# Kernel optimization log

Hardware: AMD Instinct MI355X
Metric: run time of the kernel (lower is better)

## Reference

```python
import jax, jax.numpy as jnp
import numpy as np

B, CD, NF, V, D = 16384, 13, 26, 100000, 64
BOT = [256, 128]
TOP = [512, 256, 128]
NUM_EMB = NF + 1            # 27 (bottom output + 26 categorical)
NUM_INTER = NUM_EMB * (NUM_EMB - 1) // 2  # 351
TOP_IN = NUM_INTER + NUM_EMB * D          # 2079
BN_INV = 1.0 / np.sqrt(1.0 + 1e-5)        # eval-mode BatchNorm: running_mean=0, running_var=1


def _lin(key, fan_in, fan_out):
    kw, kb = jax.random.split(key)
    s = 1.0 / np.sqrt(fan_in)
    W = jax.random.uniform(kw, (fan_in, fan_out), minval=-s, maxval=s, dtype=jnp.float32)
    b = jax.random.uniform(kb, (fan_out,), minval=-s, maxval=s, dtype=jnp.float32)
    return W, b


def setup_inputs() -> dict:
    key = jax.random.key(0)
    ks = jax.random.split(key, 16)
    continuous = jax.random.normal(ks[0], (B, CD), dtype=jnp.float32)
    cat_idx = jax.random.randint(ks[1], (B, NF), 0, V, dtype=jnp.int32)
    emb_tables = jax.random.normal(ks[2], (NF, V, D), dtype=jnp.float32)  # nn.Embedding init ~ N(0,1)
    W1, b1 = _lin(ks[3], CD, BOT[0]);   g1 = jnp.ones((BOT[0],)); be1 = jnp.zeros((BOT[0],))
    W2, b2 = _lin(ks[4], BOT[0], BOT[1]); g2 = jnp.ones((BOT[1],)); be2 = jnp.zeros((BOT[1],))
    W3, b3 = _lin(ks[5], BOT[1], D)
    W4, b4 = _lin(ks[6], TOP_IN, TOP[0]); g4 = jnp.ones((TOP[0],)); be4 = jnp.zeros((TOP[0],))
    W5, b5 = _lin(ks[7], TOP[0], TOP[1]); g5 = jnp.ones((TOP[1],)); be5 = jnp.zeros((TOP[1],))
    W6, b6 = _lin(ks[8], TOP[1], TOP[2]); g6 = jnp.ones((TOP[2],)); be6 = jnp.zeros((TOP[2],))
    W7, b7 = _lin(ks[9], TOP[2], 1)
    return dict(continuous=continuous, cat_idx=cat_idx, emb_tables=emb_tables,
                W1=W1, b1=b1, g1=g1, be1=be1, W2=W2, b2=b2, g2=g2, be2=be2, W3=W3, b3=b3,
                W4=W4, b4=b4, g4=g4, be4=be4, W5=W5, b5=b5, g5=g5, be5=be5,
                W6=W6, b6=b6, g6=g6, be6=be6, W7=W7, b7=b7)


def _bn(x, g, b):
    # eval-mode BatchNorm1d with running_mean=0, running_var=1
    return g * (x * BN_INV) + b


def reference(continuous, cat_idx, emb_tables,
              W1, b1, g1, be1, W2, b2, g2, be2, W3, b3,
              W4, b4, g4, be4, W5, b5, g5, be5, W6, b6, g6, be6, W7, b7):
    # Bottom MLP: 13 -> 256 -> 128 -> 64
    h = jax.nn.relu(_bn(continuous @ W1 + b1, g1, be1))
    h = jax.nn.relu(_bn(h @ W2 + b2, g2, be2))
    bottom = h @ W3 + b3                         # [B, D]

    # Embedding gather: one table per categorical feature
    emb = emb_tables[jnp.arange(NF), cat_idx]    # [B, NF, D]
    all_emb = jnp.concatenate([bottom[:, None, :], emb], axis=1)  # [B, 27, D]

    # Pairwise dot-product interactions via one bmm + triu gather
    Z = jnp.einsum('bnd,bmd->bnm', all_emb, all_emb)              # [B, 27, 27]
    iu, ju = np.triu_indices(NUM_EMB, k=1)                        # row-major i<j (matches torch loop order)
    inter = Z[:, iu, ju]                                          # [B, 351]

    top_in = jnp.concatenate([inter, all_emb.reshape(all_emb.shape[0], -1)], axis=1)  # [B, 2079]

    # Top MLP: 2079 -> 512 -> 256 -> 128 -> 1
    t = jax.nn.relu(_bn(top_in @ W4 + b4, g4, be4))
    t = jax.nn.relu(_bn(t @ W5 + b5, g5, be5))
    t = jax.nn.relu(_bn(t @ W6 + b6, g6, be6))
    scores = t @ W7 + b7                                          # [B, 1]
    return scores
```

## Files before the change

### kernel.cpp

```cpp
#include <hip/hip_runtime.h>
#include <stdint.h>
#include <stddef.h>

#define BATCH   16384
#define CDIM    13
#define NFEAT   26
#define VROWS   100000
#define EDIM    64
#define NEMB    27
#define NINTER  351
#define TOPIN   2079
#define KP4     2112
#define BN_INVF 0.9999950000374997f

typedef __attribute__((ext_vector_type(8)))  __bf16 bf16x8;
typedef __attribute__((ext_vector_type(4)))  float  f32x4;
typedef __attribute__((ext_vector_type(16))) float  f32x16;
typedef __attribute__((ext_vector_type(4)))  uint32_t uint4v;

__device__ __forceinline__ uint32_t f2bf(float f){
  uint32_t u = __float_as_uint(f);
  return (u + 0x7fffu + ((u >> 16) & 1u)) >> 16;
}
__device__ __forceinline__ float bf2f(uint32_t h){ return __uint_as_float(h << 16); }
__device__ __forceinline__ uint32_t pack2(float a, float b){
  return f2bf(a) | (f2bf(b) << 16);
}
__device__ __forceinline__ void async_load16(const void* g, void* l){
  __builtin_amdgcn_global_load_lds(
      (const __attribute__((address_space(1))) uint32_t*)g,
      (__attribute__((address_space(3))) uint32_t*)l, 16, 0, 0);
}
__device__ __forceinline__ int rswz(int row){ return ((row ^ (row >> 3)) & 7) << 3; }

__device__ __forceinline__ void transpose_tile(
    float (*tile)[65], const float* __restrict__ src, unsigned short* __restrict__ dst,
    int K, int N, int Kpad, int remap, int kb, int nb){
  int k0 = kb*64, n0 = nb*64, t = threadIdx.x;
  int srcBase = remap ? ((k0 < 1728) ? (k0 + 351) : (k0 - 1728)) : k0;
  #pragma unroll 4
  for(int p = 0; p < 16; p++){
    int kr = p*4 + (t >> 6), nc = t & 63;
    float v = 0.f;
    if(k0 + kr < K && (n0 + nc) < N) v = src[(size_t)(srcBase + kr) * N + n0 + nc];
    tile[kr][nc] = v;
  }
  __syncthreads();
  #pragma unroll 4
  for(int p = 0; p < 16; p++){
    int nr = p*4 + (t >> 6), kc = t & 63;
    if(k0 + kc < Kpad && (n0 + nr) < N)
      dst[(size_t)(n0 + nr) * Kpad + k0 + kc] = (unsigned short)f2bf(tile[kc][nr]);
  }
}

__global__ __launch_bounds__(256) void prep(
    const float* __restrict__ W1, const float* __restrict__ W2, const float* __restrict__ W3,
    const float* __restrict__ W4, const float* __restrict__ W5, const float* __restrict__ W6,
    unsigned short* __restrict__ W1t, unsigned short* __restrict__ W2t,
    unsigned short* __restrict__ W3t, unsigned short* __restrict__ W4t,
    unsigned short* __restrict__ W5t, unsigned short* __restrict__ W6t){
  __shared__ float tile[64][65];
  int bid = blockIdx.x;
  if(bid < 264){ transpose_tile(tile, W4, W4t, TOPIN, 512, KP4, 1, bid % 33, bid / 33); }
  else if(bid < 296){ int r = bid-264; transpose_tile(tile, W5, W5t, 512, 256, 512, 0, r % 8, r / 8); }
  else if(bid < 304){ int r = bid-296; transpose_tile(tile, W6, W6t, 256, 128, 256, 0, r % 4, r / 4); }
  else if(bid < 312){ int r = bid-304; transpose_tile(tile, W2, W2t, 256, 128, 256, 0, r % 4, r / 4); }
  else if(bid < 314){ int r = bid-312; transpose_tile(tile, W3, W3t, 128, 64, 128, 0, r, 0); }
  else               { int r = bid-314; transpose_tile(tile, W1, W1t, CDIM, 256, 32, 0, 0, r); }
}

__global__ __launch_bounds__(256) void bottom_interact(
    const float* __restrict__ cont, const int* __restrict__ cat_idx,
    const float* __restrict__ emb,
    const unsigned short* __restrict__ W1t, const unsigned short* __restrict__ W2t,
    const unsigned short* __restrict__ W3t,
    const float* __restrict__ b1, const float* __restrict__ g1, const float* __restrict__ be1,
    const float* __restrict__ b2, const float* __restrict__ g2, const float* __restrict__ be2,
    const float* __restrict__ b3,
    unsigned short* __restrict__ top_in){
  __shared__ unsigned short h1hi[16*256];
  __shared__ unsigned short h1lo[16*256];
  __shared__ unsigned short h2hi[16*128];
  __shared__ unsigned short h2lo[16*128];
  __shared__ unsigned short bot_s[16*64];
  __shared__ unsigned short inter_s[16][352];
  int t = threadIdx.x, w = t >> 6, l = t & 63;
  int m0 = blockIdx.x * 16;
  int lr = l & 15, lg = l >> 4, lk = lg * 8;
  int r = l & 31, h = l >> 5;
  bool activeB = (r >= 1 && r < NEMB);

  int idx4[4];
  #pragma unroll
  for(int s = 0; s < 4; s++){
    int b = m0 + w*4 + s;
    idx4[s] = activeB ? cat_idx[b*NFEAT + (r-1)] : 0;
  }

  bf16x8 axh, axl;
  {
    uint32_t uh[4], ul[4];
    #pragma unroll
    for(int p = 0; p < 4; p++){
      float x0 = 0.f, x1 = 0.f;
      int k0 = lk + 2*p;
      if(k0 < CDIM)     x0 = cont[(size_t)(m0 + lr)*CDIM + k0];
      if(k0 + 1 < CDIM) x1 = cont[(size_t)(m0 + lr)*CDIM + k0 + 1];
      uint32_t h0 = f2bf(x0), h1b = f2bf(x1);
      uh[p] = h0 | (h1b << 16);
      ul[p] = f2bf(x0 - bf2f(h0)) | (f2bf(x1 - bf2f(h1b)) << 16);
    }
    uint4v vh, vl;
    #pragma unroll
    for(int e = 0; e < 4; e++){ vh[e] = uh[e]; vl[e] = ul[e]; }
    axh = __builtin_bit_cast(bf16x8, vh);
    axl = __builtin_bit_cast(bf16x8, vl);
  }

  {
    #pragma unroll
    for(int nt = 0; nt < 4; nt++){
      int n = w*64 + nt*16 + lr;
      bf16x8 bw = *(const bf16x8*)(W1t + (size_t)n*32 + lk);
      f32x4 acc;
      #pragma unroll
      for(int e = 0; e < 4; e++) acc[e] = 0.f;
      acc = __builtin_amdgcn_mfma_f32_16x16x32_bf16(axh, bw, acc, 0, 0, 0);
      acc = __builtin_amdgcn_mfma_f32_16x16x32_bf16(axl, bw, acc, 0, 0, 0);
      float sc = g1[n]*BN_INVF, bo = be1[n], bi = b1[n];
      #pragma unroll
      for(int q = 0; q < 4; q++){
        int ro = lg*4 + q;
        float y = fmaxf(sc*(acc[q] + bi) + bo, 0.f);
        uint32_t hb = f2bf(y);
        int idx = ro*256 + (n ^ rswz(ro));
        h1hi[idx] = (unsigned short)hb;
        h1lo[idx] = (unsigned short)f2bf(y - bf2f(hb));
      }
    }
  }
  __syncthreads();

  {
    f32x4 acc[2];
    #pragma unroll
    for(int nt = 0; nt < 2; nt++)
      #pragma unroll
      for(int e = 0; e < 4; e++) acc[nt][e] = 0.f;
    for(int ks = 0; ks < 8; ks++){
      bf16x8 bw[2];
      #pragma unroll
      for(int nt = 0; nt < 2; nt++){
        int n = w*32 + nt*16 + lr;
        bw[nt] = *(const bf16x8*)(W2t + (size_t)n*256 + ks*32 + lk);
      }
      int ai = lr*256 + ((ks*32 + lk) ^ rswz(lr));
      bf16x8 ah = *(const bf16x8*)(h1hi + ai);
      bf16x8 al = *(const bf16x8*)(h1lo + ai);
      #pragma unroll
      for(int nt = 0; nt < 2; nt++){
        acc[nt] = __builtin_amdgcn_mfma_f32_16x16x32_bf16(ah, bw[nt], acc[nt], 0, 0, 0);
        acc[nt] = __builtin_amdgcn_mfma_f32_16x16x32_bf16(al, bw[nt], acc[nt], 0, 0, 0);
      }
    }
    #pragma unroll
    for(int nt = 0; nt < 2; nt++){
      int n = w*32 + nt*16 + lr;
      float sc = g2[n]*BN_INVF, bo = be2[n], bi = b2[n];
      #pragma unroll
      for(int q = 0; q < 4; q++){
        int ro = lg*4 + q;
        float y = fmaxf(sc*(acc[nt][q] + bi) + bo, 0.f);
        uint32_t hb = f2bf(y);
        int idx = ro*128 + (n ^ rswz(ro));
        h2hi[idx] = (unsigned short)hb;
        h2lo[idx] = (unsigned short)f2bf(y - bf2f(hb));
      }
    }
  }
  __syncthreads();

  {
    f32x4 acc;
    #pragma unroll
    for(int e = 0; e < 4; e++) acc[e] = 0.f;
    int n = w*16 + lr;
    for(int ks = 0; ks < 4; ks++){
      bf16x8 bw = *(const bf16x8*)(W3t + (size_t)n*128 + ks*32 + lk);
      int ai = lr*128 + ((ks*32 + lk) ^ rswz(lr));
      bf16x8 ah = *(const bf16x8*)(h2hi + ai);
      bf16x8 al = *(const bf16x8*)(h2lo + ai);
      acc = __builtin_amdgcn_mfma_f32_16x16x32_bf16(ah, bw, acc, 0, 0, 0);
      acc = __builtin_amdgcn_mfma_f32_16x16x32_bf16(al, bw, acc, 0, 0, 0);
    }
    float bi = b3[n];
    #pragma unroll
    for(int q = 0; q < 4; q++){
      int ro = lg*4 + q;
      bot_s[ro*64 + n] = (unsigned short)f2bf(acc[q] + bi);
    }
  }
  __syncthreads();

  float4 raw[8];
  if(activeB){
    const float* src = emb + ((size_t)(r-1)*VROWS + (size_t)idx4[0])*64;
    #pragma unroll
    for(int p = 0; p < 4; p++){
      raw[2*p]   = *(const float4*)(src + h*8 + p*16);
      raw[2*p+1] = *(const float4*)(src + h*8 + p*16 + 4);
    }
  }
  #pragma unroll
  for(int s = 0; s < 4; s++){
    int sb = w*4 + s;
    int b = m0 + sb;
    uint4v q[4];
    if(r == 0){
      #pragma unroll
      for(int p = 0; p < 4; p++)
        q[p] = *(const uint4v*)(bot_s + sb*64 + h*8 + p*16);
    } else if(activeB){
      #pragma unroll
      for(int p = 0; p < 4; p++){
        q[p][0] = pack2(raw[2*p].x, raw[2*p].y); q[p][1] = pack2(raw[2*p].z, raw[2*p].w);
        q[p][2] = pack2(raw[2*p+1].x, raw[2*p+1].y); q[p][3] = pack2(raw[2*p+1].z, raw[2*p+1].w);
      }
    } else {
      #pragma unroll
      for(int p = 0; p < 4; p++){ q[p][0]=0; q[p][1]=0; q[p][2]=0; q[p][3]=0; }
    }
    if(s < 3 && activeB){
      const float* src = emb + ((size_t)(r-1)*VROWS + (size_t)idx4[s+1])*64;
      #pragma unroll
      for(int p = 0; p < 4; p++){
        raw[2*p]   = *(const float4*)(src + h*8 + p*16);
        raw[2*p+1] = *(const float4*)(src + h*8 + p*16 + 4);
      }
    }
    if(r < NEMB){
      #pragma unroll
      for(int p = 0; p < 4; p++)
        *(uint4v*)(top_in + (size_t)b*KP4 + r*64 + h*8 + p*16) = q[p];
    }
    f32x16 acc;
    #pragma unroll
    for(int i = 0; i < 16; i++) acc[i] = 0.f;
    #pragma unroll
    for(int p = 0; p < 4; p++){
      bf16x8 a = __builtin_bit_cast(bf16x8, q[p]);
      acc = __builtin_amdgcn_mfma_f32_32x32x16_bf16(a, a, acc, 0, 0, 0);
    }
    if(r < NEMB){
      #pragma unroll
      for(int qq = 0; qq < 16; qq++){
        int i = (qq & 3) + 8*(qq >> 2) + 4*h;
        if(i < r){
          int p = i*(53 - i)/2 + (r - i - 1);
          inter_s[sb][p] = (unsigned short)f2bf(acc[qq]);
        }
      }
    }
    asm volatile("s_waitcnt lgkmcnt(0)" ::: "memory");
    size_t basei = (size_t)b*KP4 + 1728;
    for(int t0 = l; t0 < 176; t0 += 64){
      uint32_t lo = inter_s[sb][2*t0];
      uint32_t hi = (2*t0 + 1 < NINTER) ? (uint32_t)inter_s[sb][2*t0 + 1] : 0u;
      *(uint32_t*)(top_in + basei + 2*t0) = lo | (hi << 16);
    }
    if(l < 16) *(uint32_t*)(top_in + (size_t)b*KP4 + 2080 + 2*l) = 0;
  }
}

template<int KSTEPS, int NB>
__global__ __launch_bounds__(512, 2) void gemm_deep(
    const unsigned short* __restrict__ A, int sA,
    const unsigned short* __restrict__ Bw, int sB,
    const float* __restrict__ bias, const float* __restrict__ gg,
    const float* __restrict__ be,
    unsigned short* __restrict__ out, int sOut){
  __shared__ char smem[3*49152];
  int nwg = gridDim.x;
  int bid = blockIdx.x;
  int lin = (bid & 7) * (nwg >> 3) + (bid >> 3);
  int m0 = (lin / NB) * 256, n0 = (lin % NB) * 128;
  int t = threadIdx.x, w = t >> 6, l = t & 63;
  int wr = (w >> 1) * 64, wc = (w & 1) * 64;
  f32x4 acc[4][4];
  #pragma unroll
  for(int i = 0; i < 4; i++)
    #pragma unroll
    for(int j = 0; j < 4; j++)
      #pragma unroll
      for(int e = 0; e < 4; e++) acc[i][j][e] = 0.f;

  const unsigned short* g[6];
  int ldsOff[6];
  #pragma unroll
  for(int i = 0; i < 6; i++){
    if(i < 4){
      int o = i*8192 + t*16;
      int row = o >> 7;
      int cb  = (o & 127) ^ ((row & 7) << 4);
      g[i] = A + (size_t)(m0 + row)*sA + (cb >> 1);
      ldsOff[i] = o;
    } else {
      int o = (i-4)*8192 + t*16;
      int row = o >> 7;
      int cb  = (o & 127) ^ ((row & 7) << 4);
      g[i] = Bw + (size_t)(n0 + row)*sB + (cb >> 1);
      ldsOff[i] = 32768 + o;
    }
  }
  int lr = l & 15;
  int o1 = ((l >> 4) * 16) ^ ((l & 7) << 4);

  #pragma unroll
  for(int i = 0; i < 6; i++) async_load16(g[i], smem + ldsOff[i]);
  #pragma unroll
  for(int i = 0; i < 6; i++) async_load16(g[i] + 64, smem + 49152 + ldsOff[i]);
  asm volatile("s_waitcnt vmcnt(6)" ::: "memory");
  __builtin_amdgcn_s_barrier();

  for(int kt = 0; kt < KSTEPS; kt++){
    int cur = kt % 3;
    int nxt2 = (kt + 2) % 3;
    int ksrc = (kt + 2 < KSTEPS) ? (kt + 2) : (KSTEPS - 1);
    const char* bA = smem + cur*49152;
    const char* bB = bA + 32768;
    #pragma unroll
    for(int i = 0; i < 3; i++)
      async_load16(g[i] + ksrc*64, smem + nxt2*49152 + ldsOff[i]);
    {
      bf16x8 af[4], bfr[4];
      #pragma unroll
      for(int x = 0; x < 4; x++){
        af[x]  = *(const bf16x8*)(bA + (wr + x*16 + lr)*128 + o1);
        bfr[x] = *(const bf16x8*)(bB + (wc + x*16 + lr)*128 + o1);
      }
      __builtin_amdgcn_s_barrier();
      __builtin_amdgcn_s_setprio(1);
      #pragma unroll
      for(int tr = 0; tr < 4; tr++)
        #pragma unroll
        for(int tc = 0; tc < 4; tc++)
          acc[tr][tc] = __builtin_amdgcn_mfma_f32_16x16x32_bf16(af[tr], bfr[tc], acc[tr][tc], 0, 0, 0);
      __builtin_amdgcn_s_setprio(0);
    }
    __builtin_amdgcn_s_barrier();
    #pragma unroll
    for(int i = 3; i < 6; i++)
      async_load16(g[i] + ksrc*64, smem + nxt2*49152 + ldsOff[i]);
    {
      bf16x8 af[4], bfr[4];
      int ko = o1 ^ 64;
      #pragma unroll
      for(int x = 0; x < 4; x++){
        af[x]  = *(const bf16x8*)(bA + (wr + x*16 + lr)*128 + ko);
        bfr[x] = *(const bf16x8*)(bB + (wc + x*16 + lr)*128 + ko);
      }
      asm volatile("s_waitcnt vmcnt(6)" ::: "memory");
      __builtin_amdgcn_s_barrier();
      __builtin_amdgcn_s_setprio(1);
      #pragma unroll
      for(int tr = 0; tr < 4; tr++)
        #pragma unroll
        for(int tc = 0; tc < 4; tc++)
          acc[tr][tc] = __builtin_amdgcn_mfma_f32_16x16x32_bf16(af[tr], bfr[tc], acc[tr][tc], 0, 0, 0);
      __builtin_amdgcn_s_setprio(0);
    }
    __builtin_amdgcn_s_barrier();
  }

  #pragma unroll
  for(int tc = 0; tc < 4; tc++){
    int n = n0 + wc + tc*16 + lr;
    float sc = gg[n]*BN_INVF, bo = be[n], bi = bias[n];
    #pragma unroll
    for(int tr = 0; tr < 4; tr++){
      int mb = m0 + wr + tr*16 + (l >> 4)*4;
      #pragma unroll
      for(int qq = 0; qq < 4; qq++){
        float y = fmaxf(sc*(acc[tr][tc][qq] + bi) + bo, 0.f);
        out[(size_t)(mb + qq)*sOut + n] = (unsigned short)f2bf(y);
      }
    }
  }
}

__global__ __launch_bounds__(256) void gemm_tail(
    const unsigned short* __restrict__ h4,
    const unsigned short* __restrict__ W5t,
    const float* __restrict__ b5, const float* __restrict__ g5, const float* __restrict__ be5,
    const unsigned short* __restrict__ W6t,
    const float* __restrict__ b6, const float* __restrict__ g6, const float* __restrict__ be6,
    const float* __restrict__ W7, const float* __restrict__ b7,
    float* __restrict__ scores){
  __shared__ char smem[74752];
  unsigned short* h5 = (unsigned short*)(smem + 40960);
  float* pscore = (float*)(smem + 73728);
  int t = threadIdx.x, w = t >> 6, l = t & 63;
  int m0 = blockIdx.x * 64;
  int lr = l & 15;
  int o1 = ((l >> 4) * 16) ^ ((l & 7) << 4);

  f32x4 acc5[4][4];
  #pragma unroll
  for(int i = 0; i < 4; i++)
    #pragma unroll
    for(int j = 0; j < 4; j++)
      #pragma unroll
      for(int e = 0; e < 4; e++) acc5[i][j][e] = 0.f;

  const unsigned short* gA[2]; int ldsA[2];
  #pragma unroll
  for(int i = 0; i < 2; i++){
    int o = i*4096 + t*16;
    int row = o >> 7;
    int cb = (o & 127) ^ ((row & 7) << 4);
    gA[i] = h4 + (size_t)(m0 + row)*512 + (cb >> 1);
    ldsA[i] = o;
  }
  const unsigned short* gB[8]; int ldsB[8];
  #pragma unroll
  for(int i = 0; i < 8; i++){
    int o = i*4096 + t*16;
    int row = o >> 7;
    int cb = (o & 127) ^ ((row & 7) << 4);
    gB[i] = W5t + (size_t)row*512 + (cb >> 1);
    ldsB[i] = 8192 + o;
  }

  for(int kt = 0; kt < 8; kt++){
    #pragma unroll
    for(int i = 0; i < 2; i++) async_load16(gA[i] + kt*64, smem + ldsA[i]);
    #pragma unroll
    for(int i = 0; i < 8; i++) async_load16(gB[i] + kt*64, smem + ldsB[i]);
    __syncthreads();
    #pragma unroll
    for(int ks = 0; ks < 2; ks++){
      int ko = o1 ^ (ks << 6);
      bf16x8 af[4], bfr[4];
      #pragma unroll
      for(int x = 0; x < 4; x++){
        af[x]  = *(const bf16x8*)(smem + (x*16 + lr)*128 + ko);
        bfr[x] = *(const bf16x8*)(smem + 8192 + (w*64 + x*16 + lr)*128 + ko);
      }
      #pragma unroll
      for(int tr = 0; tr < 4; tr++)
        #pragma unroll
        for(int tc = 0; tc < 4; tc++)
          acc5[tr][tc] = __builtin_amdgcn_mfma_f32_16x16x32_bf16(af[tr], bfr[tc], acc5[tr][tc], 0, 0, 0);
    }
    __syncthreads();
  }

  #pragma unroll
  for(int i = 0; i < 8; i++){
    int o = i*4096 + t*16;
    int row = o >> 8;
    int cb = (o & 255) ^ ((row & 15) << 4);
    async_load16(W6t + (size_t)row*256 + (cb >> 1), smem + o);
  }
  #pragma unroll
  for(int tc = 0; tc < 4; tc++){
    int c = w*64 + tc*16 + lr;
    float sc = g5[c]*BN_INVF, bo = be5[c], bi = b5[c];
    #pragma unroll
    for(int tr = 0; tr < 4; tr++){
      #pragma unroll
      for(int qq = 0; qq < 4; qq++){
        int row = tr*16 + (l >> 4)*4 + qq;
        float y = fmaxf(sc*(acc5[tr][tc][qq] + bi) + bo, 0.f);
        h5[row*256 + (c ^ rswz(row))] = (unsigned short)f2bf(y);
      }
    }
  }
  __syncthreads();

  f32x4 acc6[4][2];
  #pragma unroll
  for(int i = 0; i < 4; i++)
    #pragma unroll
    for(int j = 0; j < 2; j++)
      #pragma unroll
      for(int e = 0; e < 4; e++) acc6[i][j][e] = 0.f;
  int lk = (l >> 4) * 8;
  int lk2 = (l >> 4) * 16;
  #pragma unroll
  for(int half = 0; half < 2; half++){
    if(half == 1){
      __syncthreads();
      #pragma unroll
      for(int i = 0; i < 8; i++){
        int o = i*4096 + t*16;
        int row = o >> 8;
        int cb = (o & 255) ^ ((row & 15) << 4);
        async_load16(W6t + (size_t)row*256 + 128 + (cb >> 1), smem + o);
      }
      __syncthreads();
    }
    #pragma unroll
    for(int ks = 0; ks < 4; ks++){
      bf16x8 af6[4], bfr6[2];
      #pragma unroll
      for(int mt = 0; mt < 4; mt++){
        int row = mt*16 + lr;
        af6[mt] = *(const bf16x8*)(h5 + row*256 + ((half*128 + ks*32 + lk) ^ rswz(row)));
      }
      #pragma unroll
      for(int nt = 0; nt < 2; nt++){
        int row = w*32 + nt*16 + lr;
        bfr6[nt] = *(const bf16x8*)(smem + row*256 + ((ks*64 + lk2) ^ (lr << 4)));
      }
      #pragma unroll
      for(int mt = 0; mt < 4; mt++)
        #pragma unroll
        for(int nt = 0; nt < 2; nt++)
          acc6[mt][nt] = __builtin_amdgcn_mfma_f32_16x16x32_bf16(af6[mt], bfr6[nt], acc6[mt][nt], 0, 0, 0);
    }
  }

  float pr[16];
  #pragma unroll
  for(int nt = 0; nt < 2; nt++){
    int c = w*32 + nt*16 + lr;
    float sc = g6[c]*BN_INVF, bo = be6[c], bi = b6[c];
    float w7c = W7[c];
    #pragma unroll
    for(int mt = 0; mt < 4; mt++){
      #pragma unroll
      for(int qq = 0; qq < 4; qq++){
        float v = fmaxf(sc*(acc6[mt][nt][qq] + bi) + bo, 0.f) * w7c;
        if(nt == 0) pr[mt*4 + qq] = v; else pr[mt*4 + qq] += v;
      }
    }
  }
  #pragma unroll
  for(int mask = 1; mask < 16; mask <<= 1){
    #pragma unroll
    for(int i = 0; i < 16; i++) pr[i] += __shfl_xor(pr[i], mask, 64);
  }
  if(lr == 0){
    #pragma unroll
    for(int mt = 0; mt < 4; mt++)
      #pragma unroll
      for(int qq = 0; qq < 4; qq++)
        pscore[w*64 + mt*16 + (l >> 4)*4 + qq] = pr[mt*4 + qq];
  }
  __syncthreads();
  if(t < 64){
    float s = b7[0] + pscore[t] + pscore[64 + t] + pscore[128 + t] + pscore[192 + t];
    scores[m0 + t] = s;
  }
}

static inline size_t alignup(size_t x){ return (x + 255) & ~(size_t)255; }

extern "C" void kernel_launch(void* const* d_in, const int* in_sizes, int n_in,
                              void* d_out, int out_size, void* d_ws, size_t ws_size,
                              hipStream_t stream){
  const float* cont = (const float*)d_in[0];
  const int*   cat  = (const int*)  d_in[1];
  const float* emb  = (const float*)d_in[2];
  const float* W1 = (const float*)d_in[3],  *b1 = (const float*)d_in[4];
  const float* g1 = (const float*)d_in[5],  *be1= (const float*)d_in[6];
  const float* W2 = (const float*)d_in[7],  *b2 = (const float*)d_in[8];
  const float* g2 = (const float*)d_in[9],  *be2= (const float*)d_in[10];
  const float* W3 = (const float*)d_in[11], *b3 = (const float*)d_in[12];
  const float* W4 = (const float*)d_in[13], *b4 = (const float*)d_in[14];
  const float* g4 = (const float*)d_in[15], *be4= (const float*)d_in[16];
  const float* W5 = (const float*)d_in[17], *b5 = (const float*)d_in[18];
  const float* g5 = (const float*)d_in[19], *be5= (const float*)d_in[20];
  const float* W6 = (const float*)d_in[21], *b6 = (const float*)d_in[22];
  const float* g6 = (const float*)d_in[23], *be6= (const float*)d_in[24];
  const float* W7 = (const float*)d_in[25], *b7 = (const float*)d_in[26];

  char* ws = (char*)d_ws;
  unsigned short* W1t  = (unsigned short*)ws; ws += alignup((size_t)256*32*2);
  unsigned short* W2t  = (unsigned short*)ws; ws += alignup((size_t)128*256*2);
  unsigned short* W3t  = (unsigned short*)ws; ws += alignup((size_t)64*128*2);
  unsigned short* topi = (unsigned short*)ws; ws += alignup((size_t)BATCH*KP4*2);
  unsigned short* W4t  = (unsigned short*)ws; ws += alignup((size_t)512*KP4*2);
  unsigned short* W5t  = (unsigned short*)ws; ws += alignup((size_t)256*512*2);
  unsigned short* W6t  = (unsigned short*)ws; ws += alignup((size_t)128*256*2);
  unsigned short* h4   = (unsigned short*)ws; ws += alignup((size_t)BATCH*512*2);
  (void)ws_size; (void)n_in; (void)in_sizes; (void)out_size;

  hipLaunchKernelGGL(prep, dim3(318), dim3(256), 0, stream,
                     W1, W2, W3, W4, W5, W6,
                     W1t, W2t, W3t, W4t, W5t, W6t);
  hipLaunchKernelGGL(bottom_interact, dim3(BATCH/16), dim3(256), 0, stream,
                     cont, cat, emb, W1t, W2t, W3t,
                     b1, g1, be1, b2, g2, be2, b3, topi);
  hipLaunchKernelGGL((gemm_deep<33, 4>), dim3(256), dim3(512), 0, stream,
                     topi, KP4, W4t, KP4, b4, g4, be4, h4, 512);
  hipLaunchKernelGGL(gemm_tail, dim3(256), dim3(256), 0, stream,
                     h4, W5t, b5, g5, be5, W6t, b6, g6, be6, W7, b7, (float*)d_out);
}
```

Baseline: 116.4 us.

## Fuse embedding gather into top GEMM and drop materialized top_in buffer

Stops writing the full bf16 top_in matrix. The bottom kernel now emits only the bottom-MLP output and padded interaction vectors. The first top-layer GEMM builds its A tiles directly: bottom, fp32 embedding rows gathered and packed to bf16, then interactions, staged through registers into LDS. The pipeline also moves from a 3-stage async buffer to a 2-stage register-staged double buffer. This avoids a large intermediate write and read, but each embedding row is gathered once per N tile (four times) and latency from the irregular gathers sits inside the GEMM main loop.

```diff
diff --git a/kernel.cpp b/kernel.cpp
--- a/kernel.cpp
+++ b/kernel.cpp
@@ -78,7 +78,7 @@
     const float* __restrict__ b1, const float* __restrict__ g1, const float* __restrict__ be1,
     const float* __restrict__ b2, const float* __restrict__ g2, const float* __restrict__ be2,
     const float* __restrict__ b3,
-    unsigned short* __restrict__ top_in){
+    unsigned short* __restrict__ bottomBF, unsigned short* __restrict__ interP){
   __shared__ unsigned short h1hi[16*256];
   __shared__ unsigned short h1lo[16*256];
   __shared__ unsigned short h2hi[16*128];
@@ -198,7 +198,9 @@
     #pragma unroll
     for(int q = 0; q < 4; q++){
       int ro = lg*4 + q;
-      bot_s[ro*64 + n] = (unsigned short)f2bf(acc[q] + bi);
+      unsigned short v = (unsigned short)f2bf(acc[q] + bi);
+      bot_s[ro*64 + n] = v;
+      bottomBF[(size_t)(m0 + ro)*64 + n] = v;
     }
   }
   __syncthreads();
@@ -238,11 +240,6 @@
         raw[2*p]   = *(const float4*)(src + h*8 + p*16);
         raw[2*p+1] = *(const float4*)(src + h*8 + p*16 + 4);
       }
-    }
-    if(r < NEMB){
-      #pragma unroll
-      for(int p = 0; p < 4; p++)
-        *(uint4v*)(top_in + (size_t)b*KP4 + r*64 + h*8 + p*16) = q[p];
     }
     f32x16 acc;
     #pragma unroll
@@ -263,26 +260,26 @@
       }
     }
     asm volatile("s_waitcnt lgkmcnt(0)" ::: "memory");
-    size_t basei = (size_t)b*KP4 + 1728;
-    for(int t0 = l; t0 < 176; t0 += 64){
-      uint32_t lo = inter_s[sb][2*t0];
+    for(int t0 = l; t0 < 192; t0 += 64){
+      uint32_t lo = (2*t0     < NINTER) ? (uint32_t)inter_s[sb][2*t0]     : 0u;
       uint32_t hi = (2*t0 + 1 < NINTER) ? (uint32_t)inter_s[sb][2*t0 + 1] : 0u;
-      *(uint32_t*)(top_in + basei + 2*t0) = lo | (hi << 16);
-    }
-    if(l < 16) *(uint32_t*)(top_in + (size_t)b*KP4 + 2080 + 2*l) = 0;
-  }
-}
-
-template<int KSTEPS, int NB>
-__global__ __launch_bounds__(512, 2) void gemm_deep(
-    const unsigned short* __restrict__ A, int sA,
-    const unsigned short* __restrict__ Bw, int sB,
+      *(uint32_t*)(interP + (size_t)b*384 + 2*t0) = lo | (hi << 16);
+    }
+  }
+}
+
+__global__ __launch_bounds__(512, 1) void gemm_fused(
+    const float* __restrict__ emb, const int* __restrict__ cat_idx,
+    const unsigned short* __restrict__ bottomBF,
+    const unsigned short* __restrict__ interP,
+    const unsigned short* __restrict__ W4t,
     const float* __restrict__ bias, const float* __restrict__ gg,
     const float* __restrict__ be,
-    unsigned short* __restrict__ out, int sOut){
-  __shared__ char smem[3*49152];
-  int nwg = gridDim.x;
-  int bid = blockIdx.x;
+    unsigned short* __restrict__ out){
+  __shared__ char smem[2*49152 + 26624];
+  int* idx_s = (int*)(smem + 98304);
+  const int NB = 4;
+  int nwg = gridDim.x, bid = blockIdx.x;
   int lin = (bid & 7) * (nwg >> 3) + (bid >> 3);
   int m0 = (lin / NB) * 256, n0 = (lin % NB) * 128;
   int t = threadIdx.x, w = t >> 6, l = t & 63;
@@ -295,82 +292,93 @@
       #pragma unroll
       for(int e = 0; e < 4; e++) acc[i][j][e] = 0.f;
 
-  const unsigned short* g[6];
-  int ldsOff[6];
-  #pragma unroll
-  for(int i = 0; i < 6; i++){
-    if(i < 4){
-      int o = i*8192 + t*16;
-      int row = o >> 7;
-      int cb  = (o & 127) ^ ((row & 7) << 4);
-      g[i] = A + (size_t)(m0 + row)*sA + (cb >> 1);
-      ldsOff[i] = o;
-    } else {
-      int o = (i-4)*8192 + t*16;
-      int row = o >> 7;
-      int cb  = (o & 127) ^ ((row & 7) << 4);
-      g[i] = Bw + (size_t)(n0 + row)*sB + (cb >> 1);
-      ldsOff[i] = 32768 + o;
-    }
-  }
+  for(int i = t; i < 256*26; i += 512) idx_s[i] = cat_idx[(size_t)m0*26 + i];
+
+  const unsigned short* gB[2]; int ldsB[2];
+  #pragma unroll
+  for(int i = 0; i < 2; i++){
+    int o = i*8192 + t*16;
+    int row = o >> 7;
+    int cb  = (o & 127) ^ ((row & 7) << 4);
+    gB[i] = W4t + (size_t)(n0 + row)*KP4 + (cb >> 1);
+    ldsB[i] = 32768 + o;
+  }
+  int s_ = t >> 1, h_ = t & 1;
+  int wcol[4];
+  #pragma unroll
+  for(int c = 0; c < 4; c++) wcol[c] = s_*128 + ((h_*64 + c*16) ^ ((s_ & 7) << 4));
   int lr = l & 15;
   int o1 = ((l >> 4) * 16) ^ ((l & 7) << 4);
 
-  #pragma unroll
-  for(int i = 0; i < 6; i++) async_load16(g[i], smem + ldsOff[i]);
-  #pragma unroll
-  for(int i = 0; i < 6; i++) async_load16(g[i] + 64, smem + 49152 + ldsOff[i]);
-  asm volatile("s_waitcnt vmcnt(6)" ::: "memory");
-  __builtin_amdgcn_s_barrier();
-
-  for(int kt = 0; kt < KSTEPS; kt++){
-    int cur = kt % 3;
-    int nxt2 = (kt + 2) % 3;
-    int ksrc = (kt + 2 < KSTEPS) ? (kt + 2) : (KSTEPS - 1);
+  float4 rf[8];
+  uint4v rb[4];
+
+  #define ISSUE_A(ktv)                                                          \
+    if((ktv) == 0){                                                             \
+      const unsigned short* src = bottomBF + (size_t)(m0 + s_)*64 + h_*32;      \
+      _Pragma("unroll")                                                         \
+      for(int c = 0; c < 4; c++) rb[c] = *(const uint4v*)(src + c*8);           \
+    } else if((ktv) <= 26){                                                     \
+      int f = (ktv) - 1;                                                        \
+      int ix = idx_s[s_*26 + f];                                                \
+      const float* src = emb + ((size_t)f*VROWS + (size_t)ix)*64 + h_*32;       \
+      _Pragma("unroll")                                                         \
+      for(int c = 0; c < 8; c++) rf[c] = *(const float4*)(src + c*4);           \
+    } else {                                                                    \
+      const unsigned short* src = interP + (size_t)(m0 + s_)*384 + ((ktv)-27)*64 + h_*32; \
+      _Pragma("unroll")                                                         \
+      for(int c = 0; c < 4; c++) rb[c] = *(const uint4v*)(src + c*8);           \
+    }
+
+  #define WRITE_A(ktv, bufA)                                                    \
+    if((ktv) >= 1 && (ktv) <= 26){                                              \
+      _Pragma("unroll")                                                         \
+      for(int c = 0; c < 4; c++){                                               \
+        uint4v v;                                                               \
+        v[0] = pack2(rf[2*c].x, rf[2*c].y);                                     \
+        v[1] = pack2(rf[2*c].z, rf[2*c].w);                                     \
+        v[2] = pack2(rf[2*c+1].x, rf[2*c+1].y);                                 \
+        v[3] = pack2(rf[2*c+1].z, rf[2*c+1].w);                                 \
+        *(uint4v*)((bufA) + wcol[c]) = v;                                       \
+      }                                                                         \
+    } else {                                                                    \
+      _Pragma("unroll")                                                         \
+      for(int c = 0; c < 4; c++) *(uint4v*)((bufA) + wcol[c]) = rb[c];          \
+    }
+
+  #pragma unroll
+  for(int i = 0; i < 2; i++) async_load16(gB[i], smem + ldsB[i]);
+  ISSUE_A(0);
+  WRITE_A(0, smem);
+  __syncthreads();
+
+  for(int kt = 0; kt < 33; kt++){
+    int cur = kt & 1, nxt = cur ^ 1;
     const char* bA = smem + cur*49152;
     const char* bB = bA + 32768;
-    #pragma unroll
-    for(int i = 0; i < 3; i++)
-      async_load16(g[i] + ksrc*64, smem + nxt2*49152 + ldsOff[i]);
-    {
+    int knx = (kt + 1 < 33) ? kt + 1 : 32;
+    #pragma unroll
+    for(int i = 0; i < 2; i++) async_load16(gB[i] + knx*64, smem + nxt*49152 + ldsB[i]);
+    ISSUE_A(knx);
+    __builtin_amdgcn_s_setprio(1);
+    #pragma unroll
+    for(int ks = 0; ks < 2; ks++){
+      int ko = o1 ^ (ks << 6);
       bf16x8 af[4], bfr[4];
       #pragma unroll
       for(int x = 0; x < 4; x++){
-        af[x]  = *(const bf16x8*)(bA + (wr + x*16 + lr)*128 + o1);
-        bfr[x] = *(const bf16x8*)(bB + (wc + x*16 + lr)*128 + o1);
-      }
-      __builtin_amdgcn_s_barrier();
-      __builtin_amdgcn_s_setprio(1);
+        af[x]  = *(const bf16x8*)(bA + (wr + x*16 + lr)*128 + ko);
+        bfr[x] = *(const bf16x8*)(bB + (wc + x*16 + lr)*128 + ko);
+      }
       #pragma unroll
       for(int tr = 0; tr < 4; tr++)
         #pragma unroll
         for(int tc = 0; tc < 4; tc++)
           acc[tr][tc] = __builtin_amdgcn_mfma_f32_16x16x32_bf16(af[tr], bfr[tc], acc[tr][tc], 0, 0, 0);
-      __builtin_amdgcn_s_setprio(0);
-    }
-    __builtin_amdgcn_s_barrier();
-    #pragma unroll
-    for(int i = 3; i < 6; i++)
-      async_load16(g[i] + ksrc*64, smem + nxt2*49152 + ldsOff[i]);
-    {
-      bf16x8 af[4], bfr[4];
-      int ko = o1 ^ 64;
-      #pragma unroll
-      for(int x = 0; x < 4; x++){
-        af[x]  = *(const bf16x8*)(bA + (wr + x*16 + lr)*128 + ko);
-        bfr[x] = *(const bf16x8*)(bB + (wc + x*16 + lr)*128 + ko);
-      }
-      asm volatile("s_waitcnt vmcnt(6)" ::: "memory");
-      __builtin_amdgcn_s_barrier();
-      __builtin_amdgcn_s_setprio(1);
-      #pragma unroll
-      for(int tr = 0; tr < 4; tr++)
-        #pragma unroll
-        for(int tc = 0; tc < 4; tc++)
-          acc[tr][tc] = __builtin_amdgcn_mfma_f32_16x16x32_bf16(af[tr], bfr[tc], acc[tr][tc], 0, 0, 0);
-      __builtin_amdgcn_s_setprio(0);
-    }
-    __builtin_amdgcn_s_barrier();
+    }
+    __builtin_amdgcn_s_setprio(0);
+    WRITE_A(knx, (char*)smem + nxt*49152);
+    __syncthreads();
   }
 
   #pragma unroll
@@ -383,10 +391,12 @@
       #pragma unroll
       for(int qq = 0; qq < 4; qq++){
         float y = fmaxf(sc*(acc[tr][tc][qq] + bi) + bo, 0.f);
-        out[(size_t)(mb + qq)*sOut + n] = (unsigned short)f2bf(y);
-      }
-    }
-  }
+        out[(size_t)(mb + qq)*512 + n] = (unsigned short)f2bf(y);
+      }
+    }
+  }
+  #undef ISSUE_A
+  #undef WRITE_A
 }
 
 __global__ __launch_bounds__(256) void gemm_tail(
@@ -581,10 +591,11 @@
   unsigned short* W1t  = (unsigned short*)ws; ws += alignup((size_t)256*32*2);
   unsigned short* W2t  = (unsigned short*)ws; ws += alignup((size_t)128*256*2);
   unsigned short* W3t  = (unsigned short*)ws; ws += alignup((size_t)64*128*2);
-  unsigned short* topi = (unsigned short*)ws; ws += alignup((size_t)BATCH*KP4*2);
   unsigned short* W4t  = (unsigned short*)ws; ws += alignup((size_t)512*KP4*2);
   unsigned short* W5t  = (unsigned short*)ws; ws += alignup((size_t)256*512*2);
   unsigned short* W6t  = (unsigned short*)ws; ws += alignup((size_t)128*256*2);
+  unsigned short* bottomBF = (unsigned short*)ws; ws += alignup((size_t)BATCH*64*2);
+  unsigned short* interP   = (unsigned short*)ws; ws += alignup((size_t)BATCH*384*2);
   unsigned short* h4   = (unsigned short*)ws; ws += alignup((size_t)BATCH*512*2);
   (void)ws_size; (void)n_in; (void)in_sizes; (void)out_size;
 
@@ -593,9 +604,9 @@
                      W1t, W2t, W3t, W4t, W5t, W6t);
   hipLaunchKernelGGL(bottom_interact, dim3(BATCH/16), dim3(256), 0, stream,
                      cont, cat, emb, W1t, W2t, W3t,
-                     b1, g1, be1, b2, g2, be2, b3, topi);
-  hipLaunchKernelGGL((gemm_deep<33, 4>), dim3(256), dim3(512), 0, stream,
-                     topi, KP4, W4t, KP4, b4, g4, be4, h4, 512);
+                     b1, g1, be1, b2, g2, be2, b3, bottomBF, interP);
+  hipLaunchKernelGGL(gemm_fused, dim3(256), dim3(512), 0, stream,
+                     emb, cat, bottomBF, interP, W4t, b4, g4, be4, h4);
   hipLaunchKernelGGL(gemm_tail, dim3(256), dim3(256), 0, stream,
                      h4, W5t, b5, g5, be5, W6t, b6, g6, be6, W7, b7, (float*)d_out);
 }
```

Result: slower. 160.0 us (+37.5%).
